# Performance work log

Hardware: AMD Instinct MI355X
Metric: run time of the kernel (lower is better)

The kernel has to match this reference:

```python
import jax, jax.numpy as jnp
import numpy as np

N_LAYERS = 2        # f_aux_layer_num
DIM = 512           # aux_dim
HEADS = 8           # aux_attn_num
HEAD = DIM // HEADS # 64 == aux_attn_dim
FFN_H = int(DIM * 2.0)  # ffn_factor = 2.0 -> 1024
BLOCK = 64          # f_block_size n
L_BLOCKS = 32
M = BLOCK + 1       # block + router token
EPS = 1e-5
THETA = 10000.0


def rms_norm(x, w):
    return x * jax.lax.rsqrt(jnp.mean(x * x, axis=-1, keepdims=True) + EPS) * w


def rotary(x):
    # x: [b, h, s, a]; matches RotaryEmb: halves rotated with outer(t, inv_freq)
    s, a = x.shape[2], x.shape[3]
    inv_freq = (1.0 / THETA) ** (jnp.arange(0, a, 2, dtype=jnp.float32) / a)
    freqs = jnp.arange(s, dtype=jnp.float32)[:, None] * inv_freq[None, :]  # [s, a/2]
    cos, sin = jnp.cos(freqs), jnp.sin(freqs)
    x1, x2 = jnp.split(x, 2, axis=-1)
    return jnp.concatenate([x1 * cos + x2 * sin, -x1 * sin + x2 * cos], axis=-1)


def setup_inputs() -> dict:
    key = jax.random.key(0)
    ks = jax.random.split(key, 10)
    B = 2
    S = L_BLOCKS * M
    x = jax.random.normal(ks[0], (B, L_BLOCKS * BLOCK, DIM), jnp.float32)
    doc = jnp.sort(jax.random.randint(ks[1], (B, S), 0, 4, dtype=jnp.int32), axis=-1)
    w = 0.02
    return {
        "x": x,
        "doc": doc,
        "router_token": jax.random.normal(ks[2], (DIM,), jnp.float32),
        "attn_w": jax.random.normal(ks[3], (N_LAYERS, DIM, 3 * DIM), jnp.float32) * w,
        "attn_o_w": jax.random.normal(ks[4], (N_LAYERS, DIM, DIM), jnp.float32) * w,
        "ffn_up_w": jax.random.normal(ks[5], (N_LAYERS, DIM, 2 * FFN_H), jnp.float32) * w,
        "ffn_down_w": jax.random.normal(ks[6], (N_LAYERS, FFN_H, DIM), jnp.float32) * w,
        "attn_norm_w": jnp.ones((N_LAYERS, DIM), jnp.float32),
        "ffn_norm_w": jnp.ones((N_LAYERS, DIM), jnp.float32),
    }


def reference(x, doc, router_token, attn_w, attn_o_w, ffn_up_w, ffn_down_w,
              attn_norm_w, ffn_norm_w):
    b = x.shape[0]
    # insert router token after each block: [b, l, n+1, d] -> [b, s, d]
    xb = x.reshape(b, L_BLOCKS, BLOCK, DIM)
    rt = jnp.broadcast_to(router_token, (b, L_BLOCKS, 1, DIM))
    h = jnp.concatenate([xb, rt], axis=2).reshape(b, L_BLOCKS * M, DIM)
    s = h.shape[1]

    # mask_mod_1: block-causal AND same-doc
    blk = jnp.arange(s) // M
    causal = blk[:, None] >= blk[None, :]                       # [s, s]
    mask = causal[None] & (doc[:, :, None] == doc[:, None, :])  # [b, s, s]
    neg = jnp.finfo(h.dtype).min
    scale = 1.0 / jnp.sqrt(jnp.float32(HEAD))

    def split_heads(t):
        return t.reshape(b, s, HEADS, HEAD).transpose(0, 2, 1, 3)

    for i in range(N_LAYERS):
        hn = rms_norm(h, attn_norm_w[i])
        qkv = hn @ attn_w[i]                       # [b, s, 3*dim]
        q, k, v = jnp.split(qkv, 3, axis=-1)
        q, k, v = split_heads(q), split_heads(k), split_heads(v)
        q, k = rotary(q), rotary(k)
        scores = jnp.einsum('bhqa,bhka->bhqk', q, k) * scale
        scores = jnp.where(mask[:, None], scores, neg)
        attn = jax.nn.softmax(scores, axis=-1)
        o = jnp.einsum('bhqk,bhka->bhqa', attn, v)
        o = o.transpose(0, 2, 1, 3).reshape(b, s, DIM)
        h = h + o @ attn_o_w[i]
        hf = rms_norm(h, ffn_norm_w[i])
        u1, u2 = jnp.split(hf @ ffn_up_w[i], 2, axis=-1)
        h = h + (jax.nn.silu(u1) * u2) @ ffn_down_w[i]

    # keep router-token slot of each block: [b, l, d]
    return h.reshape(b, L_BLOCKS, M, DIM)[:, :, -1]
```

## Files before the change

kernel.cpp:

```cpp
#include <hip/hip_runtime.h>
#include <math.h>

#define NB 2
#define LB 32
#define BLKN 64
#define MM 65
#define SS (LB*MM)
#define DD 512
#define NH 8
#define HD 64
#define FFH 1024
#define ROWS (NB*SS)
#define WT_LS 2621440

typedef __attribute__((ext_vector_type(8))) short bf16x8;
typedef __attribute__((ext_vector_type(4))) float f32x4;

__device__ __forceinline__ unsigned short f2bf(float f) {
    union { float f; unsigned u; } v; v.f = f;
    unsigned r = (v.u + 0x7FFFu + ((v.u >> 16) & 1u)) >> 16;
    return (unsigned short)r;
}
__device__ __forceinline__ float bf2f(unsigned short u) {
    union { unsigned u; float f; } v; v.u = ((unsigned)u) << 16; return v.f;
}

__device__ __forceinline__ void gload_lds16(const unsigned short* g, unsigned short* l) {
    __builtin_amdgcn_global_load_lds((const __attribute__((address_space(1))) unsigned int*)g,
                                     (__attribute__((address_space(3))) unsigned int*)l,
                                     16, 0, 0);
}

__device__ __forceinline__ int grow_map(int r) {
    return (r >> 5) * SS + (r & 31) * MM + BLKN;
}

template <int FIRST>
__global__ __launch_bounds__(256) void rms4_k(const unsigned short* __restrict__ hsrc,
                                              const float* __restrict__ x,
                                              const float* __restrict__ rt,
                                              const float* __restrict__ w,
                                              unsigned short* __restrict__ hout,
                                              unsigned short* __restrict__ out) {
    int row = blockIdx.x * 4 + (threadIdx.x >> 6);
    int lane = threadIdx.x & 63;
    float v[8];
    if (FIRST) {
        int s = row % SS, b = row / SS;
        int l = s / MM, j = s % MM;
        const float* sp = (j < BLKN) ? x + ((size_t)(b * LB + l) * BLKN + j) * DD : rt;
        float4 a = *(const float4*)(sp + lane * 8);
        float4 bq = *(const float4*)(sp + lane * 8 + 4);
        v[0] = a.x; v[1] = a.y; v[2] = a.z; v[3] = a.w;
        v[4] = bq.x; v[5] = bq.y; v[6] = bq.z; v[7] = bq.w;
    } else {
        bf16x8 h8 = *(const bf16x8*)(hsrc + (size_t)row * DD + lane * 8);
        #pragma unroll
        for (int j = 0; j < 8; ++j) v[j] = bf2f((unsigned short)h8[j]);
    }
    float ss = 0.0f;
    #pragma unroll
    for (int j = 0; j < 8; ++j) ss += v[j] * v[j];
    #pragma unroll
    for (int off = 32; off; off >>= 1) ss += __shfl_xor(ss, off);
    float r = rsqrtf(ss * (1.0f / 512.0f) + 1e-5f);
    float4 w0 = *(const float4*)(w + lane * 8);
    float4 w1 = *(const float4*)(w + lane * 8 + 4);
    float wv[8] = {w0.x, w0.y, w0.z, w0.w, w1.x, w1.y, w1.z, w1.w};
    unsigned short o8[8];
    #pragma unroll
    for (int j = 0; j < 8; ++j) o8[j] = f2bf(v[j] * r * wv[j]);
    *(bf16x8*)(out + (size_t)row * DD + lane * 8) = *(const bf16x8*)o8;
    if (FIRST) {
        unsigned short h8[8];
        #pragma unroll
        for (int j = 0; j < 8; ++j) h8[j] = f2bf(v[j]);
        *(bf16x8*)(hout + (size_t)row * DD + lane * 8) = *(const bf16x8*)h8;
    }
}

__global__ __launch_bounds__(256) void wtrans_all_k(const float* __restrict__ attn_w,
                                                    const float* __restrict__ attn_o_w,
                                                    const float* __restrict__ up_w,
                                                    const float* __restrict__ down_w,
                                                    unsigned short* __restrict__ wt) {
    __shared__ unsigned short T[64][66];
    int wg = blockIdx.x;
    int layer = wg >= 640;
    int r = wg - layer * 640;
    const float* W; int K, N; size_t dstOff; int perm = 0;
    if (r < 192)      { W = attn_w   + (size_t)layer * 512 * 1536; K = 512;  N = 1536; dstOff = 0; }
    else if (r < 256) { W = attn_o_w + (size_t)layer * 512 * 512;  K = 512;  N = 512;  dstOff = 786432;  r -= 192; }
    else if (r < 512) { W = up_w     + (size_t)layer * 512 * 2048; K = 512;  N = 2048; dstOff = 1048576; perm = 1; r -= 256; }
    else              { W = down_w   + (size_t)layer * 1024 * 512; K = 1024; N = 512;  dstOff = 2097152; r -= 512; }
    unsigned short* dst = wt + (size_t)layer * WT_LS + dstOff;
    int ntn = N >> 6;
    int n0 = (r % ntn) * 64, k0 = (r / ntn) * 64;
    int t = threadIdx.x;
    #pragma unroll
    for (int i = 0; i < 16; ++i) {
        int e = t + i * 256;
        int rr = e >> 6, cc = e & 63;
        T[rr][cc] = f2bf(W[(size_t)(k0 + rr) * N + n0 + cc]);
    }
    __syncthreads();
    #pragma unroll
    for (int i = 0; i < 16; ++i) {
        int e = t + i * 256;
        int rr = e >> 6, cc = e & 63;
        int n = n0 + rr;
        int nr = n;
        if (perm) {
            int p = n & 1023;
            nr = ((p >> 4) << 5) | ((n >> 10) << 4) | (p & 15);
        }
        dst[(size_t)nr * K + k0 + cc] = T[cc][rr];
    }
}

__global__ __launch_bounds__(256) void vtrans_k(const unsigned short* __restrict__ qkv,
                                                unsigned short* __restrict__ vT) {
    __shared__ unsigned short T[64][72];
    int wg = blockIdx.x;
    int st = wg % 33;
    int dt = (wg / 33) % 8;
    int b = wg / (33 * 8);
    int s0 = st * 64, d0 = dt * 64;
    int t = threadIdx.x;
    #pragma unroll
    for (int it = 0; it < 2; ++it) {
        int r = (t >> 3) + it * 32;
        int dd = (t & 7) * 8;
        int s = s0 + r; if (s > SS - 1) s = SS - 1;
        bf16x8 v8 = *(const bf16x8*)(qkv + ((size_t)(b * SS + s)) * 1536 + 1024 + d0 + dd);
        #pragma unroll
        for (int j = 0; j < 8; ++j) T[dd + j][r] = ((unsigned short*)&v8)[j];
    }
    __syncthreads();
    #pragma unroll
    for (int it = 0; it < 2; ++it) {
        int d = (t >> 3) + it * 32;
        int sc = (t & 7) * 8;
        int s = s0 + sc;
        if (s < SS)
            *(bf16x8*)(vT + (size_t)(b * 512 + d0 + d) * SS + s) = *(const bf16x8*)&T[d][sc];
    }
}

template <int ADD, int OBF, int ROPE, int SILU>
__global__ __launch_bounds__(256) void gemm128_k(const unsigned short* __restrict__ A,
                                                 const unsigned short* __restrict__ Wt,
                                                 void* __restrict__ Cp,
                                                 int K, int N, int colOff) {
    __shared__ unsigned short As[128 * 64];
    __shared__ unsigned short Bs[128 * 64];
    int t = threadIdx.x;
    int lane = t & 63, wv = t >> 6;
    int wm = wv >> 1, wn = wv & 1;
    int rowBase = blockIdx.y * 128, colBase = blockIdx.x * 128;
    int c = lane & 15, g = lane >> 4;
    int sw = (c & 7) << 4;

    f32x4 acc[4][4];
    #pragma unroll
    for (int mt = 0; mt < 4; ++mt)
        #pragma unroll
        for (int nt = 0; nt < 4; ++nt) { f32x4 z = {0, 0, 0, 0}; acc[mt][nt] = z; }

    for (int k0 = 0; k0 < K; k0 += 64) {
        __syncthreads();
        #pragma unroll
        for (int i = 0; i < 4; ++i) {
            int e0 = (i * 4 + wv) * 64;
            int e = e0 + lane;
            int row = e >> 3;
            int kb = ((e & 7) << 4) ^ ((row & 7) << 4);
            int gr = rowBase + row; if (gr > ROWS - 1) gr = ROWS - 1;
            gload_lds16(A + (size_t)gr * K + k0 + (kb >> 1), &As[e0 * 8]);
        }
        #pragma unroll
        for (int i = 0; i < 4; ++i) {
            int e0 = (i * 4 + wv) * 64;
            int e = e0 + lane;
            int row = e >> 3;
            int kb = ((e & 7) << 4) ^ ((row & 7) << 4);
            gload_lds16(Wt + (size_t)(colOff + colBase + row) * K + k0 + (kb >> 1), &Bs[e0 * 8]);
        }
        __syncthreads();

        bf16x8 af[4][2], bfr[4][2];
        #pragma unroll
        for (int mt = 0; mt < 4; ++mt)
            #pragma unroll
            for (int hf = 0; hf < 2; ++hf)
                af[mt][hf] = *(const bf16x8*)
                    &As[((wm * 64 + mt * 16 + c) * 128 + ((hf * 64 + g * 16) ^ sw)) >> 1];
        #pragma unroll
        for (int nt = 0; nt < 4; ++nt)
            #pragma unroll
            for (int hf = 0; hf < 2; ++hf)
                bfr[nt][hf] = *(const bf16x8*)
                    &Bs[((wn * 64 + nt * 16 + c) * 128 + ((hf * 64 + g * 16) ^ sw)) >> 1];
        __builtin_amdgcn_s_setprio(1);
        #pragma unroll
        for (int mt = 0; mt < 4; ++mt)
            #pragma unroll
            for (int nt = 0; nt < 4; ++nt) {
                acc[mt][nt] = __builtin_amdgcn_mfma_f32_16x16x32_bf16(af[mt][0], bfr[nt][0], acc[mt][nt], 0, 0, 0);
                acc[mt][nt] = __builtin_amdgcn_mfma_f32_16x16x32_bf16(af[mt][1], bfr[nt][1], acc[mt][nt], 0, 0, 0);
            }
        __builtin_amdgcn_s_setprio(0);
    }

    if (ROPE) {
        int sec = (colOff + colBase + wn * 64) >> 9;
        if (sec < 2) {
            #pragma unroll
            for (int mt = 0; mt < 4; ++mt)
                #pragma unroll
                for (int j = 0; j < 4; ++j) {
                    int row = rowBase + wm * 64 + mt * 16 + g * 4 + j;
                    int spos = row % SS;
                    #pragma unroll
                    for (int p = 0; p < 2; ++p) {
                        float jj = (float)(c + p * 16);
                        float inv = exp2f(jj * -0.41524101186092030f);
                        float fr = (float)spos * inv;
                        float sn, cs; __sincosf(fr, &sn, &cs);
                        float a = acc[mt][p][j], bb = acc[mt][p + 2][j];
                        acc[mt][p][j] = a * cs + bb * sn;
                        acc[mt][p + 2][j] = -a * sn + bb * cs;
                    }
                }
        }
    }

    #pragma unroll
    for (int mt = 0; mt < 4; ++mt)
        #pragma unroll
        for (int j = 0; j < 4; ++j) {
            int row = rowBase + wm * 64 + mt * 16 + g * 4 + j;
            if (row >= ROWS) continue;
            if (SILU) {
                unsigned short* gr = (unsigned short*)Cp + (size_t)row * 1024;
                #pragma unroll
                for (int ntp = 0; ntp < 2; ++ntp) {
                    int npr = colBase + wn * 64 + ntp * 32;
                    int p = ((npr >> 5) << 4) + c;
                    float u1 = acc[mt][2 * ntp][j];
                    float u2 = acc[mt][2 * ntp + 1][j];
                    gr[p] = f2bf((u1 / (1.0f + __expf(-u1))) * u2);
                }
            } else {
                size_t off = (size_t)row * N + colOff + colBase + wn * 64 + c;
                if (OBF) {
                    unsigned short* cr = (unsigned short*)Cp + off;
                    #pragma unroll
                    for (int nt = 0; nt < 4; ++nt) cr[nt * 16] = f2bf(acc[mt][nt][j]);
                } else {
                    float* cr = (float*)Cp + off;
                    #pragma unroll
                    for (int nt = 0; nt < 4; ++nt) {
                        if (ADD) cr[nt * 16] += acc[mt][nt][j];
                        else     cr[nt * 16] = acc[mt][nt][j];
                    }
                }
            }
        }
}

template <int MODE, int ADD>
__global__ __launch_bounds__(256) void gemm64_k(const unsigned short* __restrict__ A,
                                                const unsigned short* __restrict__ Wt,
                                                void* __restrict__ Cp,
                                                const unsigned short* __restrict__ Hsrc,
                                                float* __restrict__ outp,
                                                int K, int N) {
    __shared__ unsigned short As[64 * 64];
    __shared__ unsigned short Bs[128 * 64];
    int t = threadIdx.x;
    int lane = t & 63, wv = t >> 6;
    int wm = wv >> 1, wn = wv & 1;
    int rowBase = blockIdx.y * 64, colBase = blockIdx.x * 128;
    int c = lane & 15, g = lane >> 4;
    int sw = (c & 7) << 4;

    f32x4 acc[2][4];
    #pragma unroll
    for (int mt = 0; mt < 2; ++mt)
        #pragma unroll
        for (int nt = 0; nt < 4; ++nt) { f32x4 z = {0, 0, 0, 0}; acc[mt][nt] = z; }

    for (int k0 = 0; k0 < K; k0 += 64) {
        __syncthreads();
        #pragma unroll
        for (int i = 0; i < 2; ++i) {
            int e0 = (i * 4 + wv) * 64;
            int e = e0 + lane;
            int row = e >> 3;
            int kb = ((e & 7) << 4) ^ ((row & 7) << 4);
            int gr = rowBase + row;
            gload_lds16(A + (size_t)gr * K + k0 + (kb >> 1), &As[e0 * 8]);
        }
        #pragma unroll
        for (int i = 0; i < 4; ++i) {
            int e0 = (i * 4 + wv) * 64;
            int e = e0 + lane;
            int row = e >> 3;
            int kb = ((e & 7) << 4) ^ ((row & 7) << 4);
            gload_lds16(Wt + (size_t)(colBase + row) * K + k0 + (kb >> 1), &Bs[e0 * 8]);
        }
        __syncthreads();

        bf16x8 af[2][2], bfr[4][2];
        #pragma unroll
        for (int mt = 0; mt < 2; ++mt)
            #pragma unroll
            for (int hf = 0; hf < 2; ++hf)
                af[mt][hf] = *(const bf16x8*)
                    &As[((wm * 32 + mt * 16 + c) * 128 + ((hf * 64 + g * 16) ^ sw)) >> 1];
        #pragma unroll
        for (int nt = 0; nt < 4; ++nt)
            #pragma unroll
            for (int hf = 0; hf < 2; ++hf)
                bfr[nt][hf] = *(const bf16x8*)
                    &Bs[((wn * 64 + nt * 16 + c) * 128 + ((hf * 64 + g * 16) ^ sw)) >> 1];
        __builtin_amdgcn_s_setprio(1);
        #pragma unroll
        for (int mt = 0; mt < 2; ++mt)
            #pragma unroll
            for (int nt = 0; nt < 4; ++nt) {
                acc[mt][nt] = __builtin_amdgcn_mfma_f32_16x16x32_bf16(af[mt][0], bfr[nt][0], acc[mt][nt], 0, 0, 0);
                acc[mt][nt] = __builtin_amdgcn_mfma_f32_16x16x32_bf16(af[mt][1], bfr[nt][1], acc[mt][nt], 0, 0, 0);
            }
        __builtin_amdgcn_s_setprio(0);
    }

    #pragma unroll
    for (int mt = 0; mt < 2; ++mt)
        #pragma unroll
        for (int j = 0; j < 4; ++j) {
            int row = rowBase + wm * 32 + mt * 16 + g * 4 + j;
            int col = colBase + wn * 64 + c;
            if (MODE == 0) {
                if (ADD) {
                    unsigned short* cr = (unsigned short*)Cp + (size_t)row * N + col;
                    #pragma unroll
                    for (int nt = 0; nt < 4; ++nt)
                        cr[nt * 16] = f2bf(bf2f(cr[nt * 16]) + acc[mt][nt][j]);
                } else {
                    float* cr = (float*)Cp + (size_t)row * N + col;
                    #pragma unroll
                    for (int nt = 0; nt < 4; ++nt) cr[nt * 16] = acc[mt][nt][j];
                }
            } else if (MODE == 2) {
                int gr = grow_map(row);
                unsigned short* cr = (unsigned short*)Cp + (size_t)row * 512 + col;
                const unsigned short* hsr = Hsrc + (size_t)gr * 512 + col;
                #pragma unroll
                for (int nt = 0; nt < 4; ++nt)
                    cr[nt * 16] = f2bf(bf2f(hsr[nt * 16]) + acc[mt][nt][j]);
            } else if (MODE == 3) {
                float* cr = outp + (size_t)row * 512 + col;
                const unsigned short* hsr = Hsrc + (size_t)row * 512 + col;
                #pragma unroll
                for (int nt = 0; nt < 4; ++nt) cr[nt * 16] = bf2f(hsr[nt * 16]) + acc[mt][nt][j];
            } else {
                unsigned short* gr = (unsigned short*)Cp + (size_t)row * 1024;
                #pragma unroll
                for (int ntp = 0; ntp < 2; ++ntp) {
                    int npr = colBase + wn * 64 + ntp * 32;
                    int p = ((npr >> 5) << 4) + c;
                    float u1 = acc[mt][2 * ntp][j];
                    float u2 = acc[mt][2 * ntp + 1][j];
                    gr[p] = f2bf((u1 / (1.0f + __expf(-u1))) * u2);
                }
            }
        }
}

#define QR 80

__global__ __launch_bounds__(320) void attn_mfma_k(const unsigned short* __restrict__ qkv,
                                                   const unsigned short* __restrict__ vT,
                                                   const int* __restrict__ doc,
                                                   unsigned short* __restrict__ o) {
    __shared__ unsigned short QP[5760];
    __shared__ unsigned short Ks[2][64 * 64];
    __shared__ unsigned short Vs[2][64 * 64];
    __shared__ int docq[QR];
    __shared__ int dock[2][64];

    unsigned short* Qs = QP;
    unsigned short (*Ps)[16][72] = (unsigned short (*)[16][72])QP;

    int idx = blockIdx.x;
    int l = (idx < 256) ? (31 - (idx >> 4)) : ((idx - 256) >> 4);
    int b = (idx >> 3) & 1;
    int h = idx & 7;
    int t = threadIdx.x;
    int lane = t & 63;
    int wv = t >> 6;

    const unsigned short* qb = qkv + (size_t)b * SS * 1536;
    const unsigned short* vb = vT + (size_t)(b * 512 + h * 64) * SS;
    int rowq0 = l * MM;
    int kmax = (l + 1) * MM;

    #pragma unroll
    for (int it = 0; it < 2; ++it) {
        int ebase = it * 320 + wv * 64;
        int e = ebase + lane;
        int row = e >> 3;
        int kb = ((e & 7) << 4) ^ ((row & 7) << 4);
        int gr = rowq0 + row; if (gr > SS - 1) gr = SS - 1;
        gload_lds16(qb + (size_t)gr * 1536 + h * 64 + (kb >> 1), &Qs[ebase * 8]);
    }
    if (t < QR) docq[t] = (t < MM) ? doc[b * SS + rowq0 + t] : -999999;

    int d0 = doc[b * SS + rowq0];
    int lo = 0, hi = rowq0;
    while (lo < hi) {
        int mid = (lo + hi) >> 1;
        if (doc[b * SS + mid] < d0) lo = mid + 1; else hi = mid;
    }
    int kts = lo >> 6;
    int nkt = (kmax + 63) >> 6;

    const int mt = wv;
    const int g = lane >> 4;
    const int c = lane & 15;
    const int sw = (c & 7) << 4;

    auto stageK = [&](int kbase, int buf) {
        int ebase = wv * 64;
        int e = ebase + lane;
        int row = e >> 3;
        int kb = ((e & 7) << 4) ^ ((row & 7) << 4);
        int kg = kbase + row; if (kg > kmax - 1) kg = kmax - 1;
        gload_lds16(qb + (size_t)kg * 1536 + 512 + h * 64 + (kb >> 1), &Ks[buf][ebase * 8]);
        if (wv < 3) {
            int eb2 = 320 + wv * 64;
            int e2 = eb2 + lane;
            int row2 = e2 >> 3;
            int kb2 = ((e2 & 7) << 4) ^ ((row2 & 7) << 4);
            int kg2 = kbase + row2; if (kg2 > kmax - 1) kg2 = kmax - 1;
            gload_lds16(qb + (size_t)kg2 * 1536 + 512 + h * 64 + (kb2 >> 1), &Ks[buf][eb2 * 8]);
        }
    };
    auto stageV = [&](int kbase, int buf) {
        int ebase = wv * 64;
        int e = ebase + lane;
        int d = e >> 3;
        int kb = ((e & 7) << 4) ^ ((d & 7) << 4);
        gload_lds16(vb + (size_t)d * SS + kbase + (kb >> 1), &Vs[buf][ebase * 8]);
        if (wv < 3) {
            int eb2 = 320 + wv * 64;
            int e2 = eb2 + lane;
            int d2 = e2 >> 3;
            int kb2 = ((e2 & 7) << 4) ^ ((d2 & 7) << 4);
            gload_lds16(vb + (size_t)d2 * SS + kbase + (kb2 >> 1), &Vs[buf][eb2 * 8]);
        }
    };

    stageK(kts << 6, 0);
    stageV(kts << 6, 0);
    if (t < 64) {
        int kg = (kts << 6) + t;
        dock[0][t] = (kg < kmax) ? doc[b * SS + kg] : -1000000;
    }
    __syncthreads();

    bf16x8 aq[2];
    #pragma unroll
    for (int hf = 0; hf < 2; ++hf)
        aq[hf] = *(const bf16x8*)&Qs[((mt * 16 + c) * 128 + ((hf * 64 + g * 16) ^ sw)) >> 1];
    int dq[4];
    #pragma unroll
    for (int j = 0; j < 4; ++j) dq[j] = docq[mt * 16 + g * 4 + j];
    __syncthreads();

    f32x4 oacc[4];
    float m_[4], l_[4];
    #pragma unroll
    for (int nt = 0; nt < 4; ++nt) { f32x4 z = {0,0,0,0}; oacc[nt] = z; }
    #pragma unroll
    for (int j = 0; j < 4; ++j) { m_[j] = -1e30f; l_[j] = 0.0f; }

    for (int kt = kts; kt < nkt; ++kt) {
        int cur = (kt - kts) & 1;
        bool more = (kt + 1 < nkt);
        int dnx = 0;
        if (more) {
            stageK((kt + 1) << 6, cur ^ 1);
            stageV((kt + 1) << 6, cur ^ 1);
            if (t < 64) {
                int kg = ((kt + 1) << 6) + t;
                dnx = (kg < kmax) ? doc[b * SS + kg] : -1000000;
            }
        }

        f32x4 s[4];
        __builtin_amdgcn_s_setprio(1);
        #pragma unroll
        for (int sub = 0; sub < 4; ++sub) {
            f32x4 acc = {0, 0, 0, 0};
            #pragma unroll
            for (int hf = 0; hf < 2; ++hf) {
                bf16x8 bk = *(const bf16x8*)
                    &Ks[cur][((sub * 16 + c) * 128 + ((hf * 64 + g * 16) ^ sw)) >> 1];
                acc = __builtin_amdgcn_mfma_f32_16x16x32_bf16(aq[hf], bk, acc, 0, 0, 0);
            }
            s[sub] = acc;
        }
        __builtin_amdgcn_s_setprio(0);
        #pragma unroll
        for (int sub = 0; sub < 4; ++sub) {
            int dk = dock[cur][sub * 16 + c];
            #pragma unroll
            for (int j = 0; j < 4; ++j)
                s[sub][j] = (dq[j] == dk) ? s[sub][j] * 0.125f : -1e30f;
        }
        float mx[4];
        #pragma unroll
        for (int j = 0; j < 4; ++j)
            mx[j] = fmaxf(fmaxf(s[0][j], s[1][j]), fmaxf(s[2][j], s[3][j]));
        #pragma unroll
        for (int off = 1; off < 16; off <<= 1)
            #pragma unroll
            for (int j = 0; j < 4; ++j) mx[j] = fmaxf(mx[j], __shfl_xor(mx[j], off));
        float mn[4], sc[4], rs[4];
        #pragma unroll
        for (int j = 0; j < 4; ++j) {
            mn[j] = fmaxf(m_[j], mx[j]);
            sc[j] = __expf(m_[j] - mn[j]);
            m_[j] = mn[j];
            rs[j] = 0.0f;
        }
        #pragma unroll
        for (int sub = 0; sub < 4; ++sub)
            #pragma unroll
            for (int j = 0; j < 4; ++j) {
                float p = __expf(s[sub][j] - mn[j]);
                rs[j] += p;
                Ps[wv][g * 4 + j][sub * 16 + c] = f2bf(p);
            }
        #pragma unroll
        for (int off = 1; off < 16; off <<= 1)
            #pragma unroll
            for (int j = 0; j < 4; ++j) rs[j] += __shfl_xor(rs[j], off);
        #pragma unroll
        for (int j = 0; j < 4; ++j) l_[j] = l_[j] * sc[j] + rs[j];
        #pragma unroll
        for (int nt = 0; nt < 4; ++nt)
            #pragma unroll
            for (int j = 0; j < 4; ++j) oacc[nt][j] *= sc[j];
        __builtin_amdgcn_s_setprio(1);
        #pragma unroll
        for (int hf = 0; hf < 2; ++hf) {
            bf16x8 af = *(const bf16x8*)&Ps[wv][c][hf * 32 + g * 8];
            #pragma unroll
            for (int nt = 0; nt < 4; ++nt) {
                bf16x8 bv = *(const bf16x8*)
                    &Vs[cur][((nt * 16 + c) * 128 + ((hf * 64 + g * 16) ^ sw)) >> 1];
                oacc[nt] = __builtin_amdgcn_mfma_f32_16x16x32_bf16(af, bv, oacc[nt], 0, 0, 0);
            }
        }
        __builtin_amdgcn_s_setprio(0);

        if (more && t < 64) dock[cur ^ 1][t] = dnx;
        __syncthreads();
    }

    #pragma unroll
    for (int j = 0; j < 4; ++j) {
        int row = mt * 16 + g * 4 + j;
        if (row < MM) {
            float invl = 1.0f / l_[j];
            #pragma unroll
            for (int nt = 0; nt < 4; ++nt)
                o[(size_t)(b * SS + rowq0 + row) * DD + h * 64 + nt * 16 + c] =
                    f2bf(oacc[nt][j] * invl);
        }
    }
}

__global__ __launch_bounds__(256) void rattn_k(const unsigned short* __restrict__ hnb,
                                               const unsigned short* __restrict__ qkv,
                                               const unsigned short* __restrict__ wq,
                                               const int* __restrict__ doc,
                                               unsigned short* __restrict__ obr) {
    __shared__ float hn_r[DD];
    __shared__ float qs[HD];
    __shared__ float sc[SS];
    __shared__ float red_m[4], red_s[4];
    __shared__ float pacc[4][HD];

    int idx = blockIdx.x;
    int b = idx >> 8, h = (idx >> 5) & 7, l = idx & 31;
    int t = threadIdx.x;
    int lane = t & 63, wv = t >> 6;

    const unsigned short* qb = qkv + (size_t)b * SS * 1536;
    int spos = l * MM + BLKN;
    int rowq = b * SS + spos;
    int kmax = (l + 1) * MM;

    {
        unsigned v = *(const unsigned*)(hnb + (size_t)rowq * DD + t * 2);
        hn_r[t * 2] = bf2f((unsigned short)(v & 0xffff));
        hn_r[t * 2 + 1] = bf2f((unsigned short)(v >> 16));
    }
    int dr = doc[rowq];
    int lo = 0, hi = spos;
    while (lo < hi) {
        int mid = (lo + hi) >> 1;
        if (doc[b * SS + mid] < dr) lo = mid + 1; else hi = mid;
    }
    __syncthreads();

    {
        float part = 0.0f;
        const unsigned short* wr = wq + (size_t)(h * 64 + lane) * DD + wv * 128;
        #pragma unroll
        for (int k8 = 0; k8 < 16; ++k8) {
            bf16x8 w8 = *(const bf16x8*)(wr + k8 * 8);
            #pragma unroll
            for (int j = 0; j < 8; ++j)
                part += hn_r[wv * 128 + k8 * 8 + j] * bf2f((unsigned short)w8[j]);
        }
        pacc[wv][lane] = part;
    }
    __syncthreads();
    if (wv == 0) {
        float dq = pacc[0][lane] + pacc[1][lane] + pacc[2][lane] + pacc[3][lane];
        float other = __shfl_xor(dq, 32);
        float jj = (float)(lane & 31);
        float inv = exp2f(jj * -0.41524101186092030f);
        float fr = (float)spos * inv;
        float sn, cs; __sincosf(fr, &sn, &cs);
        float q1 = (lane < 32) ? dq : other;
        float q2 = (lane < 32) ? other : dq;
        qs[lane] = (lane < 32) ? (q1 * cs + q2 * sn) : (-q1 * sn + q2 * cs);
    }
    __syncthreads();

    int dc = lane & 7, k8 = lane >> 3;
    float mx = -1e30f;
    for (int k0 = lo; k0 < kmax; k0 += 32) {
        int k = k0 + wv * 8 + k8;
        float d = 0.0f;
        if (k < kmax) {
            bf16x8 kv = *(const bf16x8*)(qb + (size_t)k * 1536 + 512 + h * 64 + dc * 8);
            #pragma unroll
            for (int j = 0; j < 8; ++j)
                d += bf2f((unsigned short)kv[j]) * qs[dc * 8 + j];
        }
        #pragma unroll
        for (int off = 1; off < 8; off <<= 1) d += __shfl_xor(d, off);
        if (k < kmax) {
            float s = d * 0.125f;
            if (dc == 0) sc[k] = s;
            mx = fmaxf(mx, s);
        }
    }
    #pragma unroll
    for (int off = 32; off; off >>= 1) mx = fmaxf(mx, __shfl_xor(mx, off));
    if (lane == 0) red_m[wv] = mx;
    __syncthreads();
    mx = fmaxf(fmaxf(red_m[0], red_m[1]), fmaxf(red_m[2], red_m[3]));

    float sum = 0.0f;
    for (int k = lo + t; k < kmax; k += 256) {
        float p = __expf(sc[k] - mx);
        sc[k] = p;
        sum += p;
    }
    #pragma unroll
    for (int off = 32; off; off >>= 1) sum += __shfl_xor(sum, off);
    if (lane == 0) red_s[wv] = sum;
    __syncthreads();
    sum = red_s[0] + red_s[1] + red_s[2] + red_s[3];

    float a0 = 0, a1 = 0, a2 = 0, a3 = 0;
    int k = lo + wv;
    for (; k + 12 < kmax; k += 16) {
        a0 += sc[k]      * bf2f(qb[(size_t)k * 1536 + 1024 + h * 64 + lane]);
        a1 += sc[k + 4]  * bf2f(qb[(size_t)(k + 4) * 1536 + 1024 + h * 64 + lane]);
        a2 += sc[k + 8]  * bf2f(qb[(size_t)(k + 8) * 1536 + 1024 + h * 64 + lane]);
        a3 += sc[k + 12] * bf2f(qb[(size_t)(k + 12) * 1536 + 1024 + h * 64 + lane]);
    }
    for (; k < kmax; k += 4)
        a0 += sc[k] * bf2f(qb[(size_t)k * 1536 + 1024 + h * 64 + lane]);
    pacc[wv][lane] = (a0 + a1) + (a2 + a3);
    __syncthreads();
    if (wv == 0) {
        float o = (pacc[0][lane] + pacc[1][lane] + pacc[2][lane] + pacc[3][lane]) / sum;
        obr[(size_t)(b * LB + l) * DD + h * 64 + lane] = f2bf(o);
    }
}

extern "C" void kernel_launch(void* const* d_in, const int* in_sizes, int n_in,
                              void* d_out, int out_size, void* d_ws, size_t ws_size,
                              hipStream_t stream) {
    const float* x           = (const float*)d_in[0];
    const int*   doc         = (const int*)d_in[1];
    const float* rt          = (const float*)d_in[2];
    const float* attn_w      = (const float*)d_in[3];
    const float* attn_o_w    = (const float*)d_in[4];
    const float* ffn_up_w    = (const float*)d_in[5];
    const float* ffn_down_w  = (const float*)d_in[6];
    const float* attn_norm_w = (const float*)d_in[7];
    const float* ffn_norm_w  = (const float*)d_in[8];
    float* out = (float*)d_out;

    unsigned short* hb   = (unsigned short*)d_ws;
    unsigned short* qkvb = hb + (size_t)ROWS * 512;
    unsigned short* wt   = qkvb + (size_t)ROWS * 1536;
    unsigned short* hnb  = wt + (size_t)2 * WT_LS;
    unsigned short* ob   = hnb + (size_t)ROWS * 512;
    unsigned short* gb   = ob + (size_t)ROWS * 512;
    unsigned short* obr  = gb + (size_t)ROWS * 1024;
    unsigned short* hnr  = obr + 64 * 512;
    unsigned short* gbr  = hnr + 64 * 512;
    unsigned short* hr   = gbr + 64 * 1024;
    unsigned short* vTb  = hr + 64 * 512;

    wtrans_all_k<<<1280, 256, 0, stream>>>(attn_w, attn_o_w, ffn_up_w, ffn_down_w, wt);

    rms4_k<1><<<ROWS / 4, 256, 0, stream>>>(hb, x, rt, attn_norm_w, hb, hnb);
    gemm128_k<0, 1, 1, 0><<<dim3(12, 33), 256, 0, stream>>>(hnb, wt, qkvb, 512, 1536, 0);
    vtrans_k<<<NB * 8 * 33, 256, 0, stream>>>(qkvb, vTb);
    attn_mfma_k<<<512, 320, 0, stream>>>(qkvb, vTb, doc, ob);
    gemm64_k<0, 1><<<dim3(4, 65), 256, 0, stream>>>(ob, wt + 786432, hb, nullptr, nullptr, 512, 512);
    rms4_k<0><<<ROWS / 4, 256, 0, stream>>>(hb, x, rt, ffn_norm_w, nullptr, hnb);
    gemm128_k<0, 0, 0, 1><<<dim3(16, 33), 256, 0, stream>>>(hnb, wt + 1048576, gb, 512, 2048, 0);
    gemm64_k<0, 1><<<dim3(4, 65), 256, 0, stream>>>(gb, wt + 2097152, hb, nullptr, nullptr, 1024, 512);

    unsigned short* wl = wt + (size_t)WT_LS;
    rms4_k<0><<<ROWS / 4, 256, 0, stream>>>(hb, x, rt, attn_norm_w + 512, nullptr, hnb);
    gemm128_k<0, 1, 1, 0><<<dim3(8, 33), 256, 0, stream>>>(hnb, wl, qkvb, 512, 1536, 512);
    rattn_k<<<512, 256, 0, stream>>>(hnb, qkvb, wl, doc, obr);
    gemm64_k<2, 0><<<dim3(4, 1), 256, 0, stream>>>(obr, wl + 786432, hr, hb, nullptr, 512, 512);
    rms4_k<0><<<16, 256, 0, stream>>>(hr, x, rt, ffn_norm_w + 512, nullptr, hnr);
    gemm64_k<4, 0><<<dim3(16, 1), 256, 0, stream>>>(hnr, wl + 1048576, gbr, nullptr, nullptr, 512, 2048);
    gemm64_k<3, 0><<<dim3(4, 1), 256, 0, stream>>>(gbr, wl + 2097152, nullptr, hr, out, 1024, 512);
}
```

Baseline: 188.2 us.

## Fuse router-token layer-2 tail into one per-row GEMV kernel; vectorize weight transpose loads

Replaces the four small launches that handle the last-layer output projection, FFN norm, up-projection with SiLU gating, and down-projection for the 64 router rows with a single kernel. Each block owns one row and computes dot products against the bf16 transposed weights, keeping intermediates in shared memory. The aim is to cut launch overhead and the global round-trips between these tiny GEMMs. The cost is that every block rereads the full weight matrices, 64 blocks in total, through scalar-per-thread GEMVs with strided weight access. The weight-transpose kernel now reads float4 instead of scalars, and the now-unused epilogue modes of gemm64 are removed.

```diff
diff --git a/kernel.cpp b/kernel.cpp
--- a/kernel.cpp
+++ b/kernel.cpp
@@ -33,6 +33,21 @@
 
 __device__ __forceinline__ int grow_map(int r) {
     return (r >> 5) * SS + (r & 31) * MM + BLKN;
+}
+
+__device__ __forceinline__ float dotw(const float* v, const unsigned short* w, int K8) {
+    float a0 = 0.0f, a1 = 0.0f;
+    #pragma unroll 4
+    for (int k8 = 0; k8 < K8; k8 += 2) {
+        bf16x8 w8 = *(const bf16x8*)(w + k8 * 8);
+        bf16x8 w9 = *(const bf16x8*)(w + k8 * 8 + 8);
+        #pragma unroll
+        for (int j = 0; j < 8; ++j) {
+            a0 += v[k8 * 8 + j] * bf2f((unsigned short)w8[j]);
+            a1 += v[k8 * 8 + 8 + j] * bf2f((unsigned short)w9[j]);
+        }
+    }
+    return a0 + a1;
 }
 
 template <int FIRST>
@@ -98,10 +113,12 @@
     int n0 = (r % ntn) * 64, k0 = (r / ntn) * 64;
     int t = threadIdx.x;
     #pragma unroll
-    for (int i = 0; i < 16; ++i) {
+    for (int i = 0; i < 4; ++i) {
         int e = t + i * 256;
-        int rr = e >> 6, cc = e & 63;
-        T[rr][cc] = f2bf(W[(size_t)(k0 + rr) * N + n0 + cc]);
+        int rr = e >> 4, cc = (e & 15) * 4;
+        float4 w4 = *(const float4*)(W + (size_t)(k0 + rr) * N + n0 + cc);
+        T[rr][cc] = f2bf(w4.x); T[rr][cc + 1] = f2bf(w4.y);
+        T[rr][cc + 2] = f2bf(w4.z); T[rr][cc + 3] = f2bf(w4.w);
     }
     __syncthreads();
     #pragma unroll
@@ -342,40 +359,10 @@
         for (int j = 0; j < 4; ++j) {
             int row = rowBase + wm * 32 + mt * 16 + g * 4 + j;
             int col = colBase + wn * 64 + c;
-            if (MODE == 0) {
-                if (ADD) {
-                    unsigned short* cr = (unsigned short*)Cp + (size_t)row * N + col;
-                    #pragma unroll
-                    for (int nt = 0; nt < 4; ++nt)
-                        cr[nt * 16] = f2bf(bf2f(cr[nt * 16]) + acc[mt][nt][j]);
-                } else {
-                    float* cr = (float*)Cp + (size_t)row * N + col;
-                    #pragma unroll
-                    for (int nt = 0; nt < 4; ++nt) cr[nt * 16] = acc[mt][nt][j];
-                }
-            } else if (MODE == 2) {
-                int gr = grow_map(row);
-                unsigned short* cr = (unsigned short*)Cp + (size_t)row * 512 + col;
-                const unsigned short* hsr = Hsrc + (size_t)gr * 512 + col;
-                #pragma unroll
-                for (int nt = 0; nt < 4; ++nt)
-                    cr[nt * 16] = f2bf(bf2f(hsr[nt * 16]) + acc[mt][nt][j]);
-            } else if (MODE == 3) {
-                float* cr = outp + (size_t)row * 512 + col;
-                const unsigned short* hsr = Hsrc + (size_t)row * 512 + col;
-                #pragma unroll
-                for (int nt = 0; nt < 4; ++nt) cr[nt * 16] = bf2f(hsr[nt * 16]) + acc[mt][nt][j];
-            } else {
-                unsigned short* gr = (unsigned short*)Cp + (size_t)row * 1024;
-                #pragma unroll
-                for (int ntp = 0; ntp < 2; ++ntp) {
-                    int npr = colBase + wn * 64 + ntp * 32;
-                    int p = ((npr >> 5) << 4) + c;
-                    float u1 = acc[mt][2 * ntp][j];
-                    float u2 = acc[mt][2 * ntp + 1][j];
-                    gr[p] = f2bf((u1 / (1.0f + __expf(-u1))) * u2);
-                }
-            }
+            unsigned short* cr = (unsigned short*)Cp + (size_t)row * N + col;
+            #pragma unroll
+            for (int nt = 0; nt < 4; ++nt)
+                cr[nt * 16] = f2bf(bf2f(cr[nt * 16]) + acc[mt][nt][j]);
         }
 }
 
@@ -700,6 +687,54 @@
     }
 }
 
+__global__ __launch_bounds__(512) void rtail_k(const unsigned short* __restrict__ obr,
+                                               const unsigned short* __restrict__ hb,
+                                               const unsigned short* __restrict__ wo,
+                                               const unsigned short* __restrict__ wup,
+                                               const unsigned short* __restrict__ wdn,
+                                               const float* __restrict__ fnw,
+                                               float* __restrict__ out) {
+    __shared__ float ob_l[DD];
+    __shared__ float hf[DD];
+    __shared__ float gl[FFH];
+    __shared__ float red[8];
+
+    int r = blockIdx.x;
+    int b = r >> 5, l = r & 31;
+    size_t gr = (size_t)b * SS + l * MM + BLKN;
+    int t = threadIdx.x;
+    int lane = t & 63, wv = t >> 6;
+
+    ob_l[t] = bf2f(obr[(size_t)r * DD + t]);
+    __syncthreads();
+
+    float o = dotw(ob_l, wo + (size_t)t * DD, 64);
+    float hr = bf2f(hb[gr * DD + t]) + o;
+
+    float ss = hr * hr;
+    #pragma unroll
+    for (int off = 32; off; off >>= 1) ss += __shfl_xor(ss, off);
+    if (lane == 0) red[wv] = ss;
+    __syncthreads();
+    float tot = red[0] + red[1] + red[2] + red[3] + red[4] + red[5] + red[6] + red[7];
+    float rr = rsqrtf(tot * (1.0f / 512.0f) + 1e-5f);
+    hf[t] = hr * rr * fnw[t];
+    __syncthreads();
+
+    #pragma unroll
+    for (int i = 0; i < 2; ++i) {
+        int p = t + i * 512;
+        int nr1 = ((p >> 4) << 5) | (p & 15);
+        float u1 = dotw(hf, wup + (size_t)nr1 * DD, 64);
+        float u2 = dotw(hf, wup + (size_t)(nr1 + 16) * DD, 64);
+        gl[p] = (u1 / (1.0f + __expf(-u1))) * u2;
+    }
+    __syncthreads();
+
+    float d = dotw(gl, wdn + (size_t)t * FFH, 128);
+    out[(size_t)(b * LB + l) * DD + t] = hr + d;
+}
+
 extern "C" void kernel_launch(void* const* d_in, const int* in_sizes, int n_in,
                               void* d_out, int out_size, void* d_ws, size_t ws_size,
                               hipStream_t stream) {
@@ -721,10 +756,7 @@
     unsigned short* ob   = hnb + (size_t)ROWS * 512;
     unsigned short* gb   = ob + (size_t)ROWS * 512;
     unsigned short* obr  = gb + (size_t)ROWS * 1024;
-    unsigned short* hnr  = obr + 64 * 512;
-    unsigned short* gbr  = hnr + 64 * 512;
-    unsigned short* hr   = gbr + 64 * 1024;
-    unsigned short* vTb  = hr + 64 * 512;
+    unsigned short* vTb  = obr + 64 * 512;
 
     wtrans_all_k<<<1280, 256, 0, stream>>>(attn_w, attn_o_w, ffn_up_w, ffn_down_w, wt);
 
@@ -741,8 +773,6 @@
     rms4_k<0><<<ROWS / 4, 256, 0, stream>>>(hb, x, rt, attn_norm_w + 512, nullptr, hnb);
     gemm128_k<0, 1, 1, 0><<<dim3(8, 33), 256, 0, stream>>>(hnb, wl, qkvb, 512, 1536, 512);
     rattn_k<<<512, 256, 0, stream>>>(hnb, qkvb, wl, doc, obr);
-    gemm64_k<2, 0><<<dim3(4, 1), 256, 0, stream>>>(obr, wl + 786432, hr, hb, nullptr, 512, 512);
-    rms4_k<0><<<16, 256, 0, stream>>>(hr, x, rt, ffn_norm_w + 512, nullptr, hnr);
-    gemm64_k<4, 0><<<dim3(16, 1), 256, 0, stream>>>(hnr, wl + 1048576, gbr, nullptr, nullptr, 512, 2048);
-    gemm64_k<3, 0><<<dim3(4, 1), 256, 0, stream>>>(gbr, wl + 2097152, nullptr, hr, out, 1024, 512);
-}
+    rtail_k<<<64, 512, 0, stream>>>(obr, hb, wl + 786432, wl + 1048576, wl + 2097152,
+                                    ffn_norm_w + 512, out);
+}
```

Result: slower. 267.5 us (+42.1%).
